# Kernel tuning notes

Measured on AMD Instinct MI355X. Metric: run time of the kernel, lower is better.

## Reference

```python
import jax, jax.numpy as jnp
import numpy as np

N_NODES = 100000
N_EDGES = 1600000
D_IN, D_HID, D_OUT = 32, 64, 32


def sage_conv(x, edge_index, W_l, b_l, W_r, num_segments):
    # PyG SAGEConv (aggr='sum'): out = lin_l(sum_{j->i} x_j) + lin_r(x_i)
    src, dst = edge_index[0], edge_index[1]
    agg = jax.ops.segment_sum(x[src], dst, num_segments=num_segments)  # [N, d]
    return agg @ W_l.T + b_l + x @ W_r.T


def setup_inputs() -> dict:
    key = jax.random.key(0)
    ks = jax.random.split(key, 8)
    x = jax.random.normal(ks[0], (N_NODES, D_IN), dtype=jnp.float32)
    edge_index = jax.random.randint(ks[1], (2, N_EDGES), 0, N_NODES, dtype=jnp.int64)
    s_in = 1.0 / np.sqrt(D_IN)
    s_hid = 1.0 / np.sqrt(D_HID)
    W_l_in = jax.random.normal(ks[2], (D_HID, D_IN), dtype=jnp.float32) * s_in
    b_l_in = jnp.zeros((D_HID,), dtype=jnp.float32)
    W_r_in = jax.random.normal(ks[3], (D_HID, D_IN), dtype=jnp.float32) * s_in
    W_l_out = jax.random.normal(ks[4], (D_OUT, D_HID), dtype=jnp.float32) * s_hid
    b_l_out = jnp.zeros((D_OUT,), dtype=jnp.float32)
    W_r_out = jax.random.normal(ks[5], (D_OUT, D_HID), dtype=jnp.float32) * s_hid
    return {"x": x, "edge_index": edge_index, "W_l_in": W_l_in, "b_l_in": b_l_in,
            "W_r_in": W_r_in, "W_l_out": W_l_out, "b_l_out": b_l_out, "W_r_out": W_r_out}


def reference(x, edge_index, W_l_in, b_l_in, W_r_in, W_l_out, b_l_out, W_r_out):
    n = x.shape[0]
    h = sage_conv(x, edge_index, W_l_in, b_l_in, W_r_in, n)   # conv_in
    h = jax.nn.relu(h)                                        # act
    # dropout: identity in eval/inference mode
    out = sage_conv(h, edge_index, W_l_out, b_l_out, W_r_out, n)  # conv_out
    return out
```

## Files before the change

### kernel.cpp

```cpp
#include <hip/hip_runtime.h>


#define BLK 256
#define CAP 48
#define CCAP 18000
#define NCBMAX 104
#define STCAP 9
#define GSTRIDE 32

typedef unsigned int u32;
typedef __attribute__((ext_vector_type(8))) short b8;
typedef __attribute__((ext_vector_type(4))) float f4;
typedef __attribute__((ext_vector_type(2))) float f2v;

__device__ __forceinline__ float bflo(u32 r) { return __uint_as_float(r << 16); }
__device__ __forceinline__ float bfhi(u32 r) { return __uint_as_float(r & 0xffff0000u); }
__device__ __forceinline__ u32 bfpack(float a, float b) {
  u32 ua = __float_as_uint(a), ub = __float_as_uint(b);
  ua = (ua + 0x7fffu + ((ua >> 16) & 1u)) >> 16;
  ub = (ub + 0x7fffu + ((ub >> 16) & 1u)) & 0xffff0000u;
  return ua | ub;
}

__global__ __launch_bounds__(256) void coarse_bin(
    const int* __restrict__ ei, int* __restrict__ gcur, u32* __restrict__ grec,
    const float* __restrict__ x, u32* __restrict__ xb, u32* __restrict__ xq,
    const float* __restrict__ Wl_in, const float* __restrict__ Wr_in,
    const float* __restrict__ Wl_out, const float* __restrict__ Wr_out,
    u32* __restrict__ wf1, u32* __restrict__ wf2,
    int E, int ncb, int n8) {
  __shared__ u32 st[4][NCBMAX][STCAP];
  __shared__ int cnt[4][NCBMAX];
  __shared__ int woff[4][NCBMAX];
  __shared__ int gbase[NCBMAX];
  const int t = threadIdx.x;
  const int w = t >> 6, lane = t & 63;
  const int base = blockIdx.x << 10;
  const int nbatch = min(1024, E - base);
  for (int i = t; i < 4 * NCBMAX; i += 256) ((int*)cnt)[i] = 0;
  __syncthreads();
#pragma unroll
  for (int k = 0; k < 4; ++k) {
    int idx = (w << 8) + (k << 6) + lane;
    if (idx < nbatch) {
      int e = base + idx;
      int d = ei[E + e];
      int s = ei[e];
      int b = d >> 10;
      u32 R = ((u32)s << 10) | (u32)(d & 1023);
      int p = atomicAdd(&cnt[w][b], 1);
      if (p < STCAP) {
        st[w][b][p] = R;
      } else {
        int g = atomicAdd(&gcur[b * GSTRIDE], 1);
        if (g < CCAP) grec[(size_t)b * CCAP + g] = R;
      }
    }
  }
  __syncthreads();
  if (t < ncb) {
    int c0 = min(cnt[0][t], STCAP), c1 = min(cnt[1][t], STCAP);
    int c2 = min(cnt[2][t], STCAP), c3 = min(cnt[3][t], STCAP);
    woff[0][t] = 0; woff[1][t] = c0; woff[2][t] = c0 + c1; woff[3][t] = c0 + c1 + c2;
    gbase[t] = atomicAdd(&gcur[t * GSTRIDE], c0 + c1 + c2 + c3);
  }
  const int stride = (int)gridDim.x * 256;
  for (int i = blockIdx.x * 256 + t; i < n8; i += stride) {
    float4 f = ((const float4*)x)[i];
    xb[2 * i]     = bfpack(f.x, f.y);
    xb[2 * i + 1] = bfpack(f.z, f.w);
    int v = __builtin_amdgcn_cvt_pk_fp8_f32(f.x, f.y, 0, false);
    v     = __builtin_amdgcn_cvt_pk_fp8_f32(f.z, f.w, v, true);
    xq[i] = (u32)v;
  }
  if (blockIdx.x == 0) {
    for (int j = t; j < 2048; j += 256) {
      int p = j & 3, l = (j >> 2) & 63, tl = (j >> 8) & 3, m = j >> 10;
      const float* W = m ? Wr_in : Wl_in;
      int d = tl * 16 + (l & 15);
      int k = (l >> 4) * 8 + 2 * p;
      wf1[j] = bfpack(W[d * 32 + k], W[d * 32 + k + 1]);
    }
    for (int j = t; j < 2048; j += 256) {
      int p = j & 3, l = (j >> 2) & 63, tl = (j >> 8) & 1, c = (j >> 9) & 1, m = j >> 10;
      const float* W = m ? Wr_out : Wl_out;
      int n = tl * 16 + (l & 15);
      int k = c * 32 + (l >> 4) * 8 + 2 * p;
      wf2[j] = bfpack(W[n * 64 + k], W[n * 64 + k + 1]);
    }
  }
  __syncthreads();
  for (int i = t; i < ncb * 4 * STCAP; i += 256) {
    int b = i / (4 * STCAP), s = i % (4 * STCAP), ww = s / STCAP, p = s % STCAP;
    if (p < min(cnt[ww][b], STCAP))
      grec[(size_t)b * CCAP + gbase[b] + woff[ww][b] + p] = st[ww][b][p];
  }
}

__global__ __launch_bounds__(1024) void fine_fill(
    const int* __restrict__ gcur, const u32* __restrict__ grec,
    int* __restrict__ csr, int* __restrict__ cursor, int N) {
  __shared__ int cur[1024];
  const int b = blockIdx.x;
  const int t = threadIdx.x;
  cur[t] = 0;
  __syncthreads();
  const int len = min(gcur[b * GSTRIDE], CCAP);
  const u32* rec = grec + (size_t)b * CCAP;
  for (int i = t; i < len; i += 1024) {
    u32 R = rec[i];
    int lo = (int)(R & 1023u);
    int s = (int)(R >> 10);
    int p = atomicAdd(&cur[lo], 1);
    if (p < CAP) csr[(size_t)((b << 10) + lo) * CAP + p] = s;
  }
  __syncthreads();
  int node = (b << 10) + t;
  if (node < N) cursor[node] = cur[t];
}

__global__ __launch_bounds__(256) void mfma_fused(
    const u32* __restrict__ xq, const int* __restrict__ cnt,
    const int* __restrict__ csr, const u32* __restrict__ xb,
    const uint4* __restrict__ wf1, const uint4* __restrict__ wf2,
    const float* __restrict__ bl_in, const float* __restrict__ bl_out,
    u32* __restrict__ gb, float* __restrict__ out, int N) {
  __shared__ float sh[4][16][68];
  __shared__ u32 agg[64][20];
  const int tid = threadIdx.x;
  const int base = blockIdx.x * 64;

  {
    const int crew = tid >> 5, lane = tid & 31;
    const int gq = lane >> 2, gc = lane & 3;
    for (int r = 0; r < 8; ++r) {
      const int nl = r * 8 + crew;
      const int node = base + nl;
      if (node >= N) break;
      const int n = min(cnt[node], CAP);
      const int* row = csr + (size_t)node * CAP;
      float a0 = 0.f, a1 = 0.f, a2 = 0.f, a3 = 0.f;
      float a4 = 0.f, a5 = 0.f, a6 = 0.f, a7 = 0.f;
      int p = gq;
      for (; p + 8 < n; p += 16) {
        uint2 r0 = ((const uint2*)(xq + (size_t)row[p] * 8))[gc];
        uint2 r1 = ((const uint2*)(xq + (size_t)row[p + 8] * 8))[gc];
        f2v d;
        d = __builtin_amdgcn_cvt_pk_f32_fp8((int)r0.x, false); a0 += d.x; a1 += d.y;
        d = __builtin_amdgcn_cvt_pk_f32_fp8((int)r0.x, true);  a2 += d.x; a3 += d.y;
        d = __builtin_amdgcn_cvt_pk_f32_fp8((int)r0.y, false); a4 += d.x; a5 += d.y;
        d = __builtin_amdgcn_cvt_pk_f32_fp8((int)r0.y, true);  a6 += d.x; a7 += d.y;
        d = __builtin_amdgcn_cvt_pk_f32_fp8((int)r1.x, false); a0 += d.x; a1 += d.y;
        d = __builtin_amdgcn_cvt_pk_f32_fp8((int)r1.x, true);  a2 += d.x; a3 += d.y;
        d = __builtin_amdgcn_cvt_pk_f32_fp8((int)r1.y, false); a4 += d.x; a5 += d.y;
        d = __builtin_amdgcn_cvt_pk_f32_fp8((int)r1.y, true);  a6 += d.x; a7 += d.y;
      }
      if (p < n) {
        uint2 rr = ((const uint2*)(xq + (size_t)row[p] * 8))[gc];
        f2v d;
        d = __builtin_amdgcn_cvt_pk_f32_fp8((int)rr.x, false); a0 += d.x; a1 += d.y;
        d = __builtin_amdgcn_cvt_pk_f32_fp8((int)rr.x, true);  a2 += d.x; a3 += d.y;
        d = __builtin_amdgcn_cvt_pk_f32_fp8((int)rr.y, false); a4 += d.x; a5 += d.y;
        d = __builtin_amdgcn_cvt_pk_f32_fp8((int)rr.y, true);  a6 += d.x; a7 += d.y;
      }
#pragma unroll
      for (int off = 4; off <= 16; off <<= 1) {
        a0 += __shfl_xor(a0, off); a1 += __shfl_xor(a1, off);
        a2 += __shfl_xor(a2, off); a3 += __shfl_xor(a3, off);
        a4 += __shfl_xor(a4, off); a5 += __shfl_xor(a5, off);
        a6 += __shfl_xor(a6, off); a7 += __shfl_xor(a7, off);
      }
      if (gq == 0) {
        *(uint4*)&agg[nl][gc * 4] =
            make_uint4(bfpack(a0, a1), bfpack(a2, a3), bfpack(a4, a5), bfpack(a6, a7));
      }
    }
  }
  __syncthreads();

  const int w = tid >> 6, l = tid & 63;
  const int m = l & 15, q = l >> 4;
  const int nodeC = min(base + w * 16 + m, N - 1);

  union FU { uint4 u; b8 b; };
  FU aa, ax, h0, h1;
  aa.u = *(const uint4*)&agg[w * 16 + m][q * 4];
  ax.u = ((const uint4*)(xb + (size_t)nodeC * 16))[q];

#pragma unroll
  for (int t = 0; t < 4; ++t) {
    FU wl, wr;
    wl.u = wf1[t * 64 + l];
    wr.u = wf1[(4 + t) * 64 + l];
    float bias = bl_in[t * 16 + m];
    f4 acc = {bias, bias, bias, bias};
    acc = __builtin_amdgcn_mfma_f32_16x16x32_bf16(aa.b, wl.b, acc, 0, 0, 0);
    acc = __builtin_amdgcn_mfma_f32_16x16x32_bf16(ax.b, wr.b, acc, 0, 0, 0);
#pragma unroll
    for (int r = 0; r < 4; ++r)
      sh[w][q * 4 + r][t * 16 + m] = fmaxf(acc[r], 0.f);
  }
  __syncthreads();
  {
    float4 f0 = *(const float4*)&sh[w][m][q * 8];
    float4 f1 = *(const float4*)&sh[w][m][q * 8 + 4];
    h0.u = make_uint4(bfpack(f0.x, f0.y), bfpack(f0.z, f0.w),
                      bfpack(f1.x, f1.y), bfpack(f1.z, f1.w));
    float4 f2 = *(const float4*)&sh[w][m][32 + q * 8];
    float4 f3 = *(const float4*)&sh[w][m][32 + q * 8 + 4];
    h1.u = make_uint4(bfpack(f2.x, f2.y), bfpack(f2.z, f2.w),
                      bfpack(f3.x, f3.y), bfpack(f3.z, f3.w));
  }
  __syncthreads();
#pragma unroll
  for (int t2 = 0; t2 < 2; ++t2) {
    FU g0, g1, r0, r1;
    g0.u = wf2[(0 + t2) * 64 + l];
    g1.u = wf2[(2 + t2) * 64 + l];
    r0.u = wf2[(4 + t2) * 64 + l];
    r1.u = wf2[(6 + t2) * 64 + l];
    f4 gacc = {0.f, 0.f, 0.f, 0.f};
    gacc = __builtin_amdgcn_mfma_f32_16x16x32_bf16(h0.b, g0.b, gacc, 0, 0, 0);
    gacc = __builtin_amdgcn_mfma_f32_16x16x32_bf16(h1.b, g1.b, gacc, 0, 0, 0);
    float bias = bl_out[t2 * 16 + m];
    f4 facc = {bias, bias, bias, bias};
    facc = __builtin_amdgcn_mfma_f32_16x16x32_bf16(h0.b, r0.b, facc, 0, 0, 0);
    facc = __builtin_amdgcn_mfma_f32_16x16x32_bf16(h1.b, r1.b, facc, 0, 0, 0);
#pragma unroll
    for (int r = 0; r < 4; ++r) {
      sh[w][q * 4 + r][t2 * 16 + m] = gacc[r];
      int node = base + w * 16 + q * 4 + r;
      if (node < N) out[(size_t)node * 32 + t2 * 16 + m] = facc[r];
    }
  }
  __syncthreads();
  {
    int nl = l >> 2, cb = l & 3;
    int node = base + w * 16 + nl;
    if (node < N) {
      float4 f0 = *(const float4*)&sh[w][nl][cb * 8];
      float4 f1 = *(const float4*)&sh[w][nl][cb * 8 + 4];
      ((uint4*)(gb + (size_t)node * 16))[cb] =
          make_uint4(bfpack(f0.x, f0.y), bfpack(f0.z, f0.w),
                     bfpack(f1.x, f1.y), bfpack(f1.z, f1.w));
    }
  }
}

__global__ void gather_p2(const u32* __restrict__ feat, const int* __restrict__ cnt,
                          const int* __restrict__ csr, float* __restrict__ outp, int N) {
  int node = blockIdx.x * 8 + (threadIdx.x >> 5);
  if (node >= N) return;
  int lane = threadIdx.x & 31;
  int q = lane >> 2, c = lane & 3;
  int n = min(cnt[node], CAP);
  const int* row = csr + (size_t)node * CAP;
  float a0 = 0.f, a1 = 0.f, a2 = 0.f, a3 = 0.f;
  float a4 = 0.f, a5 = 0.f, a6 = 0.f, a7 = 0.f;
  int p = q;
  for (; p + 8 < n; p += 16) {
    int s0 = row[p];
    int s1 = row[p + 8];
    uint4 v0 = ((const uint4*)(feat + (size_t)s0 * 16))[c];
    uint4 v1 = ((const uint4*)(feat + (size_t)s1 * 16))[c];
    a0 += bflo(v0.x) + bflo(v1.x); a1 += bfhi(v0.x) + bfhi(v1.x);
    a2 += bflo(v0.y) + bflo(v1.y); a3 += bfhi(v0.y) + bfhi(v1.y);
    a4 += bflo(v0.z) + bflo(v1.z); a5 += bfhi(v0.z) + bfhi(v1.z);
    a6 += bflo(v0.w) + bflo(v1.w); a7 += bfhi(v0.w) + bfhi(v1.w);
  }
  if (p < n) {
    int s = row[p];
    uint4 v = ((const uint4*)(feat + (size_t)s * 16))[c];
    a0 += bflo(v.x); a1 += bfhi(v.x);
    a2 += bflo(v.y); a3 += bfhi(v.y);
    a4 += bflo(v.z); a5 += bfhi(v.z);
    a6 += bflo(v.w); a7 += bfhi(v.w);
  }
#pragma unroll
  for (int off = 4; off <= 16; off <<= 1) {
    a0 += __shfl_xor(a0, off); a1 += __shfl_xor(a1, off);
    a2 += __shfl_xor(a2, off); a3 += __shfl_xor(a3, off);
    a4 += __shfl_xor(a4, off); a5 += __shfl_xor(a5, off);
    a6 += __shfl_xor(a6, off); a7 += __shfl_xor(a7, off);
  }
  if (q == 0) {
    float4* o = (float4*)(outp + (size_t)node * 32 + c * 8);
    float4 p0 = o[0], p1 = o[1];
    o[0] = make_float4(p0.x + a0, p0.y + a1, p0.z + a2, p0.w + a3);
    o[1] = make_float4(p1.x + a4, p1.y + a5, p1.z + a6, p1.w + a7);
  }
}

extern "C" void kernel_launch(void* const* d_in, const int* in_sizes, int n_in,
                              void* d_out, int out_size, void* d_ws, size_t ws_size,
                              hipStream_t stream) {
  const float* x      = (const float*)d_in[0];
  const int*   ei     = (const int*)d_in[1];
  const float* Wl_in  = (const float*)d_in[2];
  const float* bl_in  = (const float*)d_in[3];
  const float* Wr_in  = (const float*)d_in[4];
  const float* Wl_out = (const float*)d_in[5];
  const float* bl_out = (const float*)d_in[6];
  const float* Wr_out = (const float*)d_in[7];
  float* out = (float*)d_out;

  const int N = in_sizes[0] / 32;
  const int E = in_sizes[1] / 2;
  const int ncb = (N + 1023) >> 10;

  u32*   ab     = (u32*)d_ws;
  int*   cursor = (int*)(ab + (size_t)N * 16);
  int*   csr    = cursor + N;
  u32*   xb     = (u32*)(csr + (size_t)N * CAP);
  u32*   gb     = xb + (size_t)N * 16;
  u32*   xq     = gb + (size_t)N * 16;
  u32*   wf1    = xq + (size_t)N * 8;
  u32*   wf2    = wf1 + 2048;
  int*   gcur   = (int*)(wf2 + 2048);
  u32*   grec   = (u32*)(gcur + (size_t)ncb * GSTRIDE);

  hipMemsetAsync(gcur, 0, (size_t)ncb * GSTRIDE * sizeof(int), stream);

  coarse_bin<<<(E + 1023) / 1024, BLK, 0, stream>>>(
      ei, gcur, grec, x, xb, xq, Wl_in, Wr_in, Wl_out, Wr_out, wf1, wf2,
      E, ncb, N * 8);
  fine_fill<<<ncb, 1024, 0, stream>>>(gcur, grec, csr, cursor, N);

  mfma_fused<<<(N + 63) / 64, 256, 0, stream>>>(xq, cursor, csr, xb,
                                                (const uint4*)wf1, (const uint4*)wf2,
                                                bl_in, bl_out, gb, out, N);
  gather_p2<<<(N + 7) / 8, 256, 0, stream>>>(gb, cursor, csr, out, N);
}
```

Baseline: 183.8 us.

## Split second-layer gather table into two column halves gathered in separate passes

```diff
diff --git a/kernel.cpp b/kernel.cpp
--- a/kernel.cpp
+++ b/kernel.cpp
@@ -124,7 +124,8 @@
     const int* __restrict__ csr, const u32* __restrict__ xb,
     const uint4* __restrict__ wf1, const uint4* __restrict__ wf2,
     const float* __restrict__ bl_in, const float* __restrict__ bl_out,
-    u32* __restrict__ gb, float* __restrict__ out, int N) {
+    u32* __restrict__ gbA, u32* __restrict__ gbB,
+    float* __restrict__ out, int N) {
   __shared__ float sh[4][16][68];
   __shared__ u32 agg[64][20];
   const int tid = threadIdx.x;
@@ -240,51 +241,41 @@
     if (node < N) {
       float4 f0 = *(const float4*)&sh[w][nl][cb * 8];
       float4 f1 = *(const float4*)&sh[w][nl][cb * 8 + 4];
-      ((uint4*)(gb + (size_t)node * 16))[cb] =
+      u32* tab = (cb < 2) ? gbA : gbB;
+      ((uint4*)(tab + (size_t)node * 8))[cb & 1] =
           make_uint4(bfpack(f0.x, f0.y), bfpack(f0.z, f0.w),
                      bfpack(f1.x, f1.y), bfpack(f1.z, f1.w));
     }
   }
 }
 
-__global__ void gather_p2(const u32* __restrict__ feat, const int* __restrict__ cnt,
-                          const int* __restrict__ csr, float* __restrict__ outp, int N) {
+__global__ void gather_half(const u32* __restrict__ feat, const int* __restrict__ cnt,
+                            const int* __restrict__ csr, float* __restrict__ outp,
+                            int off, int N) {
   int node = blockIdx.x * 8 + (threadIdx.x >> 5);
   if (node >= N) return;
   int lane = threadIdx.x & 31;
-  int q = lane >> 2, c = lane & 3;
+  int q = lane >> 1, c = lane & 1;
   int n = min(cnt[node], CAP);
   const int* row = csr + (size_t)node * CAP;
   float a0 = 0.f, a1 = 0.f, a2 = 0.f, a3 = 0.f;
   float a4 = 0.f, a5 = 0.f, a6 = 0.f, a7 = 0.f;
-  int p = q;
-  for (; p + 8 < n; p += 16) {
-    int s0 = row[p];
-    int s1 = row[p + 8];
-    uint4 v0 = ((const uint4*)(feat + (size_t)s0 * 16))[c];
-    uint4 v1 = ((const uint4*)(feat + (size_t)s1 * 16))[c];
-    a0 += bflo(v0.x) + bflo(v1.x); a1 += bfhi(v0.x) + bfhi(v1.x);
-    a2 += bflo(v0.y) + bflo(v1.y); a3 += bfhi(v0.y) + bfhi(v1.y);
-    a4 += bflo(v0.z) + bflo(v1.z); a5 += bfhi(v0.z) + bfhi(v1.z);
-    a6 += bflo(v0.w) + bflo(v1.w); a7 += bfhi(v0.w) + bfhi(v1.w);
-  }
-  if (p < n) {
-    int s = row[p];
-    uint4 v = ((const uint4*)(feat + (size_t)s * 16))[c];
+  for (int p = q; p < n; p += 16) {
+    uint4 v = ((const uint4*)(feat + (size_t)row[p] * 8))[c];
     a0 += bflo(v.x); a1 += bfhi(v.x);
     a2 += bflo(v.y); a3 += bfhi(v.y);
     a4 += bflo(v.z); a5 += bfhi(v.z);
     a6 += bflo(v.w); a7 += bfhi(v.w);
   }
 #pragma unroll
-  for (int off = 4; off <= 16; off <<= 1) {
-    a0 += __shfl_xor(a0, off); a1 += __shfl_xor(a1, off);
-    a2 += __shfl_xor(a2, off); a3 += __shfl_xor(a3, off);
-    a4 += __shfl_xor(a4, off); a5 += __shfl_xor(a5, off);
-    a6 += __shfl_xor(a6, off); a7 += __shfl_xor(a7, off);
+  for (int o = 2; o <= 16; o <<= 1) {
+    a0 += __shfl_xor(a0, o); a1 += __shfl_xor(a1, o);
+    a2 += __shfl_xor(a2, o); a3 += __shfl_xor(a3, o);
+    a4 += __shfl_xor(a4, o); a5 += __shfl_xor(a5, o);
+    a6 += __shfl_xor(a6, o); a7 += __shfl_xor(a7, o);
   }
   if (q == 0) {
-    float4* o = (float4*)(outp + (size_t)node * 32 + c * 8);
+    float4* o = (float4*)(outp + (size_t)node * 32 + off + c * 8);
     float4 p0 = o[0], p1 = o[1];
     o[0] = make_float4(p0.x + a0, p0.y + a1, p0.z + a2, p0.w + a3);
     o[1] = make_float4(p1.x + a4, p1.y + a5, p1.z + a6, p1.w + a7);
@@ -312,8 +303,9 @@
   int*   cursor = (int*)(ab + (size_t)N * 16);
   int*   csr    = cursor + N;
   u32*   xb     = (u32*)(csr + (size_t)N * CAP);
-  u32*   gb     = xb + (size_t)N * 16;
-  u32*   xq     = gb + (size_t)N * 16;
+  u32*   gbA    = xb + (size_t)N * 16;
+  u32*   gbB    = gbA + (size_t)N * 8;
+  u32*   xq     = gbB + (size_t)N * 8;
   u32*   wf1    = xq + (size_t)N * 8;
   u32*   wf2    = wf1 + 2048;
   int*   gcur   = (int*)(wf2 + 2048);
@@ -328,6 +320,7 @@
 
   mfma_fused<<<(N + 63) / 64, 256, 0, stream>>>(xq, cursor, csr, xb,
                                                 (const uint4*)wf1, (const uint4*)wf2,
-                                                bl_in, bl_out, gb, out, N);
-  gather_p2<<<(N + 7) / 8, 256, 0, stream>>>(gb, cursor, csr, out, N);
-}
+                                                bl_in, bl_out, gbA, gbB, out, N);
+  gather_half<<<(N + 7) / 8, 256, 0, stream>>>(gbA, cursor, csr, out, 0, N);
+  gather_half<<<(N + 7) / 8, 256, 0, stream>>>(gbB, cursor, csr, out, 16, N);
+}
```

Result: slower. 201.7 us (+9.8%).
